# Performance work log

Measured on AMD Instinct MI355X. Metric: run time of the kernel, lower is better.

The kernel has to match this reference:

```python
import jax, jax.numpy as jnp
import numpy as np

B, N, D, D_A, S, D_K = 512, 8192, 1024, 512, 8, 64

def setup_inputs() -> dict:
    key = jax.random.key(0)
    k1, k2, k3, k4 = jax.random.split(key, 4)
    lecun_q = 1.0 / np.sqrt(D_A)
    lecun_k = 1.0 / np.sqrt(D)
    return {
        "z": jax.random.normal(k1, (B, D_A), dtype=jnp.float32),
        "pool_vectors": jax.random.normal(k2, (N, D), dtype=jnp.float32),
        "W_Q": jax.random.normal(k3, (S, D_A, D_K), dtype=jnp.float32) * lecun_q,
        "W_K": jax.random.normal(k4, (S, D, D_K), dtype=jnp.float32) * lecun_k,
        "aspect_logits": jnp.zeros((S,), dtype=jnp.float32),
        "tau": jnp.asarray(0.5, dtype=jnp.float32),
        "lambda_sharp": jnp.asarray(10.0, dtype=jnp.float32),
        "temperature": jnp.asarray(0.1, dtype=jnp.float32),
    }

def reference(z, pool_vectors, W_Q, W_K, aspect_logits, tau, lambda_sharp, temperature):
    # Per-aspect projections
    queries = jnp.einsum('bd,adq->baq', z, W_Q)              # [B, S, d_k]
    keys = jnp.einsum('np,apq->naq', pool_vectors, W_K)       # [N, S, d_k]
    # L2 normalize along d_k
    q_norm = queries / (jnp.linalg.norm(queries, axis=-1, keepdims=True) + 1e-08)
    k_norm = keys / (jnp.linalg.norm(keys, axis=-1, keepdims=True) + 1e-08)
    # Multi-aspect cosine similarity
    sims = jnp.einsum('baq,naq->bna', q_norm, k_norm)          # [B, N, S]
    # Learned aspect weighting
    w = jax.nn.softmax(aspect_logits)                          # [S]
    scores = jnp.einsum('bna,a->bn', sims, w)                  # [B, N]
    # Sigmoid gate against threshold, temperature-scaled normalize
    g = jax.nn.sigmoid(lambda_sharp * (scores - tau))
    alpha_raw = g * jnp.exp(scores / temperature)
    alpha = alpha_raw / (jnp.sum(alpha_raw, axis=-1, keepdims=True) + 1e-08)
    return (alpha, scores, keys)
```

## Files before the change

### kernel.cpp

```cpp
#include <hip/hip_runtime.h>
#include <stdint.h>

#define B_DIM 512
#define N_DIM 8192
#define D_DIM 1024
#define DA_DIM 512
#define S_DIM 8
#define DK_DIM 64
#define C_DIM 512

typedef short v8s __attribute__((ext_vector_type(8)));
typedef float v4f __attribute__((ext_vector_type(4)));

__device__ __forceinline__ unsigned int f2bf(float x) {
    union { float f; unsigned int u; } v; v.f = x;
    unsigned int u = v.u;
    return (u + 0x7fffu + ((u >> 16) & 1u)) >> 16;
}

__device__ __forceinline__ void gld16(const unsigned short* g, unsigned short* l) {
    __builtin_amdgcn_global_load_lds(
        (const __attribute__((address_space(1))) unsigned int*)g,
        (__attribute__((address_space(3))) unsigned int*)l,
        16, 0, 0);
}

__device__ __forceinline__ void cvt8(const float* __restrict__ src,
                                     unsigned short* __restrict__ dst, int t) {
    const float4* s4 = (const float4*)src;
    float4 a = s4[2 * t], b = s4[2 * t + 1];
    uint4 o;
    o.x = f2bf(a.x) | (f2bf(a.y) << 16);
    o.y = f2bf(a.z) | (f2bf(a.w) << 16);
    o.z = f2bf(b.x) | (f2bf(b.y) << 16);
    o.w = f2bf(b.z) | (f2bf(b.w) << 16);
    ((uint4*)dst)[t] = o;
}

__device__ __forceinline__ void w_transpose_tile(const float* __restrict__ w,
                                                 unsigned short* __restrict__ wt,
                                                 int a, int dt, int ddim,
                                                 unsigned short* T ) {
    int t = threadIdx.x;
    int d0 = dt * 64;
    int kc4 = (t & 15) * 4;
    const float4* src = (const float4*)(w + ((size_t)a * ddim + d0) * DK_DIM);
    #pragma unroll
    for (int p = 0; p < 4; p++) {
        int dr = p * 16 + (t >> 4);
        float4 v = src[dr * 16 + (t & 15)];
        uint2 pk;
        pk.x = f2bf(v.x) | (f2bf(v.y) << 16);
        pk.y = f2bf(v.z) | (f2bf(v.w) << 16);
        *(uint2*)&T[dr * 68 + kc4] = pk;
    }
    __syncthreads();
    int c0 = a * 64;
    #pragma unroll
    for (int q = 0; q < 2; q++) {
        int k = q * 32 + (t >> 3);
        int ch = t & 7;
        unsigned short s[8];
        #pragma unroll
        for (int i = 0; i < 8; i++) s[i] = T[(ch * 8 + i) * 68 + k];
        uint4 o;
        o.x = (unsigned)s[0] | ((unsigned)s[1] << 16);
        o.y = (unsigned)s[2] | ((unsigned)s[3] << 16);
        o.z = (unsigned)s[4] | ((unsigned)s[5] << 16);
        o.w = (unsigned)s[6] | ((unsigned)s[7] << 16);
        *(uint4*)&wt[(size_t)(c0 + k) * ddim + d0 + ch * 8] = o;
    }
}

__global__ __launch_bounds__(256) void prep(const float* __restrict__ pool,
                                            const float* __restrict__ z,
                                            const float* __restrict__ W_Q,
                                            const float* __restrict__ W_K,
                                            unsigned short* __restrict__ poolb,
                                            unsigned short* __restrict__ zb,
                                            unsigned short* __restrict__ wqt,
                                            unsigned short* __restrict__ wtb) {
    __shared__ unsigned short T[64 * 68];
    int blk = blockIdx.x;
    if (blk < 4096) {
        cvt8(pool, poolb, blk * 256 + threadIdx.x);
    } else if (blk < 4224) {
        cvt8(z, zb, (blk - 4096) * 256 + threadIdx.x);
    } else if (blk < 4352) {
        int idx = blk - 4224;
        w_transpose_tile(W_K, wtb, idx >> 4, idx & 15, D_DIM, T);
    } else {
        int idx = blk - 4352;
        w_transpose_tile(W_Q, wqt, idx >> 3, idx & 7, DA_DIM, T);
    }
}

__device__ __forceinline__ void gemm_mainloop(const unsigned short* __restrict__ A, int lda,
                                              const unsigned short* __restrict__ Bm, int ldb,
                                              int mbase, int nbase, int kiters64,
                                              unsigned short (*As)[2][4096],
                                              unsigned short (*Bs)[2][2048],
                                              v4f acc[2][4]) {
    int tid = threadIdx.x;
    int wid = tid >> 6, lane = tid & 63;
    int quad = lane >> 4, l16 = lane & 15;
    int srow = lane >> 2;
    int scol = (lane & 3) * 8;

    auto stage = [&](int kk, int p) {
        int k0 = kk * 64;
        #pragma unroll
        for (int j = 0; j < 6; j++) {
            int i = wid * 6 + j;
            if (i < 16) {
                int c = i >> 3, g = i & 7;
                int row = g * 16 + srow;
                gld16(&A[(size_t)(mbase + row) * lda + k0 + c * 32 + scol],
                      &As[p][c][g * 512]);
            } else {
                int i2 = i - 16;
                int c = i2 >> 2, g = i2 & 3;
                int row = g * 16 + srow;
                gld16(&Bm[(size_t)(nbase + row) * ldb + k0 + c * 32 + scol],
                      &Bs[p][c][g * 512]);
            }
        }
    };

    stage(0, 0);
    for (int kk = 0; kk < kiters64; kk++) {
        __syncthreads();
        if (kk + 1 < kiters64) stage(kk + 1, (kk + 1) & 1);
        int p = kk & 1;
        #pragma unroll
        for (int c = 0; c < 2; c++) {
            v8s af[2], bf[4];
            #pragma unroll
            for (int mt = 0; mt < 2; mt++)
                af[mt] = *(const v8s*)&As[p][c][(wid * 32 + mt * 16 + l16) * 32 + quad * 8];
            #pragma unroll
            for (int nt = 0; nt < 4; nt++)
                bf[nt] = *(const v8s*)&Bs[p][c][(nt * 16 + l16) * 32 + quad * 8];
            #pragma unroll
            for (int mt = 0; mt < 2; mt++)
                #pragma unroll
                for (int nt = 0; nt < 4; nt++)
                    acc[mt][nt] = __builtin_amdgcn_mfma_f32_16x16x32_bf16(
                        af[mt], bf[nt], acc[mt][nt], 0, 0, 0);
        }
    }
}

__global__ __launch_bounds__(256, 3) void fused_gemms(const unsigned short* __restrict__ poolb,
                                                      const unsigned short* __restrict__ wtb,
                                                      const unsigned short* __restrict__ zb,
                                                      const unsigned short* __restrict__ wqt,
                                                      const float* __restrict__ logits,
                                                      float* __restrict__ keys_out,
                                                      unsigned short* __restrict__ kb,
                                                      unsigned short* __restrict__ qwb) {
    __shared__ unsigned short As[2][2][4096];
    __shared__ unsigned short Bs[2][2][2048];
    v4f acc[2][4];
    #pragma unroll
    for (int mt = 0; mt < 2; mt++)
        #pragma unroll
        for (int nt = 0; nt < 4; nt++) acc[mt][nt] = (v4f)(0.f);

    int blk = blockIdx.x;
    bool is_q = blk >= 512;
    int mbase, nbase;
    if (is_q) {
        int q = blk - 512;
        mbase = (q & 3) * 128; nbase = (q >> 2) * 64;
        gemm_mainloop(zb, DA_DIM, wqt, DA_DIM, mbase, nbase, DA_DIM / 64, As, Bs, acc);
    } else {
        mbase = (blk & 63) * 128; nbase = (blk >> 6) * 64;
        gemm_mainloop(poolb, D_DIM, wtb, D_DIM, mbase, nbase, D_DIM / 64, As, Bs, acc);
    }

    int tid = threadIdx.x, wid = tid >> 6, lane = tid & 63;
    int quad = lane >> 4, l16 = lane & 15;

    if (is_q) {
        float l[8]; float mx = -1e30f;
        #pragma unroll
        for (int i = 0; i < 8; i++) { l[i] = logits[i]; mx = fmaxf(mx, l[i]); }
        float se = 0.f;
        #pragma unroll
        for (int i = 0; i < 8; i++) { l[i] = __expf(l[i] - mx); se += l[i]; }
        float wa = l[nbase >> 6] / se;

        #pragma unroll
        for (int mt = 0; mt < 2; mt++)
            #pragma unroll
            for (int r = 0; r < 4; r++) {
                float ss = 0.f;
                #pragma unroll
                for (int nt = 0; nt < 4; nt++) ss += acc[mt][nt][r] * acc[mt][nt][r];
                ss += __shfl_xor(ss, 1, 64);
                ss += __shfl_xor(ss, 2, 64);
                ss += __shfl_xor(ss, 4, 64);
                ss += __shfl_xor(ss, 8, 64);
                float sc = wa / (sqrtf(ss) + 1e-8f);
                int row = mbase + wid * 32 + mt * 16 + quad * 4 + r;
                #pragma unroll
                for (int nt = 0; nt < 4; nt++) {
                    int col = nbase + nt * 16 + l16;
                    qwb[(size_t)row * C_DIM + col] =
                        (unsigned short)f2bf(acc[mt][nt][r] * sc);
                }
            }
    } else {
        #pragma unroll
        for (int mt = 0; mt < 2; mt++)
            #pragma unroll
            for (int r = 0; r < 4; r++) {
                float ss = 0.f;
                #pragma unroll
                for (int nt = 0; nt < 4; nt++) ss += acc[mt][nt][r] * acc[mt][nt][r];
                ss += __shfl_xor(ss, 1, 64);
                ss += __shfl_xor(ss, 2, 64);
                ss += __shfl_xor(ss, 4, 64);
                ss += __shfl_xor(ss, 8, 64);
                float sc = 1.0f / (sqrtf(ss) + 1e-8f);
                int row = mbase + wid * 32 + mt * 16 + quad * 4 + r;
                #pragma unroll
                for (int nt = 0; nt < 4; nt++) {
                    int col = nbase + nt * 16 + l16;
                    float s = acc[mt][nt][r];
                    keys_out[(size_t)row * C_DIM + col] = s;
                    kb[(size_t)row * C_DIM + col] = (unsigned short)f2bf(s * sc);
                }
            }
    }
}

__global__ __launch_bounds__(256, 3) void scores_gemm(const unsigned short* __restrict__ qwb,
                                                      const unsigned short* __restrict__ kb,
                                                      float* __restrict__ scores_out,
                                                      float* __restrict__ partials,
                                                      const float* __restrict__ lam_p,
                                                      const float* __restrict__ tau_p,
                                                      const float* __restrict__ temp_p) {
    __shared__ unsigned short As[2][2][4096];
    __shared__ unsigned short Bs[2][2][2048];
    __shared__ float rowpart[128];
    v4f acc[2][4];
    #pragma unroll
    for (int mt = 0; mt < 2; mt++)
        #pragma unroll
        for (int nt = 0; nt < 4; nt++) acc[mt][nt] = (v4f)(0.f);

    int mbase = blockIdx.y * 128, nbase = blockIdx.x * 64;
    gemm_mainloop(qwb, C_DIM, kb, C_DIM, mbase, nbase, C_DIM / 64, As, Bs, acc);

    int tid = threadIdx.x, wid = tid >> 6, lane = tid & 63;
    int quad = lane >> 4, l16 = lane & 15;

    float lam = lam_p[0], tau = tau_p[0], invT = 1.0f / temp_p[0];

    #pragma unroll
    for (int mt = 0; mt < 2; mt++)
        #pragma unroll
        for (int r = 0; r < 4; r++) {
            float rs = 0.f;
            int row = mbase + wid * 32 + mt * 16 + quad * 4 + r;
            #pragma unroll
            for (int nt = 0; nt < 4; nt++) {
                float s = acc[mt][nt][r];
                int col = nbase + nt * 16 + l16;
                scores_out[(size_t)row * N_DIM + col] = s;
                float g = 1.0f / (1.0f + __expf(-lam * (s - tau)));
                rs += g * __expf(s * invT);
            }
            rs += __shfl_xor(rs, 1, 64);
            rs += __shfl_xor(rs, 2, 64);
            rs += __shfl_xor(rs, 4, 64);
            rs += __shfl_xor(rs, 8, 64);
            if (l16 == 0)
                rowpart[wid * 32 + mt * 16 + quad * 4 + r] = rs;
        }
    __syncthreads();
    if (tid < 128)
        partials[(size_t)blockIdx.x * B_DIM + mbase + tid] = rowpart[tid];
}

__global__ __launch_bounds__(256) void alpha_kernel(const float* __restrict__ scores,
                                                    const float* __restrict__ partials,
                                                    float* __restrict__ alpha,
                                                    const float* __restrict__ lam_p,
                                                    const float* __restrict__ tau_p,
                                                    const float* __restrict__ temp_p) {
    __shared__ float red[128];
    __shared__ float s_inv;
    int b = blockIdx.x >> 1;
    int half = blockIdx.x & 1;
    int tid = threadIdx.x;
    if (tid < 128) red[tid] = partials[(size_t)tid * B_DIM + b];
    __syncthreads();
    if (tid < 64) {
        float v = red[tid] + red[tid + 64];
        v += __shfl_xor(v, 1, 64);
        v += __shfl_xor(v, 2, 64);
        v += __shfl_xor(v, 4, 64);
        v += __shfl_xor(v, 8, 64);
        v += __shfl_xor(v, 16, 64);
        v += __shfl_xor(v, 32, 64);
        if (tid == 0) s_inv = 1.0f / (v + 1e-8f);
    }
    __syncthreads();
    float inv = s_inv;
    float lam = lam_p[0], tau = tau_p[0], invT = 1.0f / temp_p[0];
    const float4* srow = (const float4*)(scores + (size_t)b * N_DIM) + half * 1024;
    float4* arow = (float4*)(alpha + (size_t)b * N_DIM) + half * 1024;
    #pragma unroll
    for (int i = 0; i < 4; i++) {
        int idx = tid + i * 256;
        float4 s4 = srow[idx];
        float4 o;
        o.x = (1.0f / (1.0f + __expf(-lam * (s4.x - tau)))) * __expf(s4.x * invT) * inv;
        o.y = (1.0f / (1.0f + __expf(-lam * (s4.y - tau)))) * __expf(s4.y * invT) * inv;
        o.z = (1.0f / (1.0f + __expf(-lam * (s4.z - tau)))) * __expf(s4.z * invT) * inv;
        o.w = (1.0f / (1.0f + __expf(-lam * (s4.w - tau)))) * __expf(s4.w * invT) * inv;
        arow[idx] = o;
    }
}

extern "C" void kernel_launch(void* const* d_in, const int* in_sizes, int n_in,
                              void* d_out, int out_size, void* d_ws, size_t ws_size,
                              hipStream_t stream) {
    const float* z      = (const float*)d_in[0];
    const float* pool   = (const float*)d_in[1];
    const float* W_Q    = (const float*)d_in[2];
    const float* W_K    = (const float*)d_in[3];
    const float* logits = (const float*)d_in[4];
    const float* tau    = (const float*)d_in[5];
    const float* lam    = (const float*)d_in[6];
    const float* temp   = (const float*)d_in[7];

    float* alpha  = (float*)d_out;
    float* scores = alpha + (size_t)B_DIM * N_DIM;
    float* keys   = scores + (size_t)B_DIM * N_DIM;

    char* ws = (char*)d_ws;
    unsigned short* poolb = (unsigned short*)(ws);
    unsigned short* kb    = (unsigned short*)(ws + 16777216);
    unsigned short* wtb   = (unsigned short*)(ws + 25165824);
    unsigned short* wqt   = (unsigned short*)(ws + 26214400);
    unsigned short* zb    = (unsigned short*)(ws + 26738688);
    unsigned short* qwb   = (unsigned short*)(ws + 27262976);
    float* partials       = (float*)(ws + 27787264);

    prep<<<dim3(4416), dim3(256), 0, stream>>>(pool, z, W_Q, W_K,
                                               poolb, zb, wqt, wtb);
    fused_gemms<<<dim3(544), dim3(256), 0, stream>>>(poolb, wtb, zb, wqt, logits,
                                                     keys, kb, qwb);
    scores_gemm<<<dim3(128, 4), dim3(256), 0, stream>>>(qwb, kb, scores, partials,
                                                        lam, tau, temp);
    alpha_kernel<<<dim3(1024), dim3(256), 0, stream>>>(scores, partials, alpha,
                                                       lam, tau, temp);
}
```

Baseline: 138.5 us.

## Fuse pool fp32-to-bf16 conversion into key GEMM A-tile loading

The separate prep pass that converted the 32MB fp32 pool into a bf16 workspace copy is removed. The key-projection GEMM now loads fp32 pool tiles into registers, converts them to bf16, and writes them to LDS, prefetching the next tile during the MFMA loop. This drops a full write and re-read of the bf16 pool. In exchange the GEMM reads twice as many bytes per A tile, uses more registers, and does conversion ALU work inside the main loop, while the pool is re-read by each of the 8 N-column blocks.

Result: slower. 158.1 us (+14.1%).

```diff
diff --git a/kernel.cpp b/kernel.cpp
--- a/kernel.cpp
+++ b/kernel.cpp
@@ -72,25 +72,21 @@
     }
 }
 
-__global__ __launch_bounds__(256) void prep(const float* __restrict__ pool,
-                                            const float* __restrict__ z,
+__global__ __launch_bounds__(256) void prep(const float* __restrict__ z,
                                             const float* __restrict__ W_Q,
                                             const float* __restrict__ W_K,
-                                            unsigned short* __restrict__ poolb,
                                             unsigned short* __restrict__ zb,
                                             unsigned short* __restrict__ wqt,
                                             unsigned short* __restrict__ wtb) {
     __shared__ unsigned short T[64 * 68];
     int blk = blockIdx.x;
-    if (blk < 4096) {
-        cvt8(pool, poolb, blk * 256 + threadIdx.x);
-    } else if (blk < 4224) {
-        cvt8(z, zb, (blk - 4096) * 256 + threadIdx.x);
-    } else if (blk < 4352) {
-        int idx = blk - 4224;
+    if (blk < 128) {
+        cvt8(z, zb, blk * 256 + threadIdx.x);
+    } else if (blk < 256) {
+        int idx = blk - 128;
         w_transpose_tile(W_K, wtb, idx >> 4, idx & 15, D_DIM, T);
     } else {
-        int idx = blk - 4352;
+        int idx = blk - 256;
         w_transpose_tile(W_Q, wqt, idx >> 3, idx & 7, DA_DIM, T);
     }
 }
@@ -151,7 +147,82 @@
     }
 }
 
-__global__ __launch_bounds__(256, 3) void fused_gemms(const unsigned short* __restrict__ poolb,
+__device__ __forceinline__ void gemm_mainloop_cvtA(const float* __restrict__ Af,
+                                                   const unsigned short* __restrict__ Bm,
+                                                   int mbase, int nbase, int kiters64,
+                                                   unsigned short (*As)[2][4096],
+                                                   unsigned short (*Bs)[2][2048],
+                                                   v4f acc[2][4]) {
+    int tid = threadIdx.x;
+    int wid = tid >> 6, lane = tid & 63;
+    int quad = lane >> 4, l16 = lane & 15;
+    int srow = lane >> 2;
+    int scol = (lane & 3) * 8;
+
+    float4 fa[4][2];
+
+    auto issueA = [&](int kk) {
+        #pragma unroll
+        for (int j = 0; j < 4; j++) {
+            int u = wid * 4 + j;
+            int c = u >> 3, g = u & 7;
+            int row = g * 16 + srow;
+            const float* p = Af + (size_t)(mbase + row) * D_DIM + kk * 64 + c * 32 + scol;
+            fa[j][0] = *(const float4*)p;
+            fa[j][1] = *(const float4*)(p + 4);
+        }
+    };
+    auto commitA = [&](int pb) {
+        #pragma unroll
+        for (int j = 0; j < 4; j++) {
+            int u = wid * 4 + j;
+            int c = u >> 3, g = u & 7;
+            uint4 o;
+            o.x = f2bf(fa[j][0].x) | (f2bf(fa[j][0].y) << 16);
+            o.y = f2bf(fa[j][0].z) | (f2bf(fa[j][0].w) << 16);
+            o.z = f2bf(fa[j][1].x) | (f2bf(fa[j][1].y) << 16);
+            o.w = f2bf(fa[j][1].z) | (f2bf(fa[j][1].w) << 16);
+            *(uint4*)&As[pb][c][g * 512 + lane * 8] = o;
+        }
+    };
+    auto gldB = [&](int kk, int pb) {
+        #pragma unroll
+        for (int j = 0; j < 2; j++) {
+            int u = wid * 2 + j;
+            int c = u >> 2, g = u & 3;
+            int row = g * 16 + srow;
+            gld16(&Bm[(size_t)(nbase + row) * D_DIM + kk * 64 + c * 32 + scol],
+                  &Bs[pb][c][g * 512]);
+        }
+    };
+
+    issueA(0); gldB(0, 0); commitA(0);
+    for (int kk = 0; kk < kiters64; kk++) {
+        __syncthreads();
+        int pn = (kk + 1) & 1;
+        if (kk + 1 < kiters64) { issueA(kk + 1); gldB(kk + 1, pn); }
+        int p = kk & 1;
+        #pragma unroll
+        for (int c = 0; c < 2; c++) {
+            v8s af[2], bf[4];
+            #pragma unroll
+            for (int mt = 0; mt < 2; mt++)
+                af[mt] = *(const v8s*)&As[p][c][(wid * 32 + mt * 16 + l16) * 32 + quad * 8];
+            #pragma unroll
+            for (int nt = 0; nt < 4; nt++)
+                bf[nt] = *(const v8s*)&Bs[p][c][(nt * 16 + l16) * 32 + quad * 8];
+            #pragma unroll
+            for (int mt = 0; mt < 2; mt++)
+                #pragma unroll
+                for (int nt = 0; nt < 4; nt++)
+                    acc[mt][nt] = __builtin_amdgcn_mfma_f32_16x16x32_bf16(
+                        af[mt], bf[nt], acc[mt][nt], 0, 0, 0);
+        }
+        if (kk + 1 < kiters64) commitA(pn);
+    }
+}
+
+__global__ __launch_bounds__(256, 3) void fused_gemms(const float* __restrict__ pool,
                                                       const unsigned short* __restrict__ wtb,
                                                       const unsigned short* __restrict__ zb,
                                                       const unsigned short* __restrict__ wqt,
@@ -176,7 +247,7 @@
         gemm_mainloop(zb, DA_DIM, wqt, DA_DIM, mbase, nbase, DA_DIM / 64, As, Bs, acc);
     } else {
         mbase = (blk & 63) * 128; nbase = (blk >> 6) * 64;
-        gemm_mainloop(poolb, D_DIM, wtb, D_DIM, mbase, nbase, D_DIM / 64, As, Bs, acc);
+        gemm_mainloop_cvtA(pool, wtb, mbase, nbase, D_DIM / 64, As, Bs, acc);
     }
 
     int tid = threadIdx.x, wid = tid >> 6, lane = tid & 63;
@@ -344,17 +415,15 @@
     float* keys   = scores + (size_t)B_DIM * N_DIM;
 
     char* ws = (char*)d_ws;
-    unsigned short* poolb = (unsigned short*)(ws);
-    unsigned short* kb    = (unsigned short*)(ws + 16777216);
-    unsigned short* wtb   = (unsigned short*)(ws + 25165824);
-    unsigned short* wqt   = (unsigned short*)(ws + 26214400);
-    unsigned short* zb    = (unsigned short*)(ws + 26738688);
-    unsigned short* qwb   = (unsigned short*)(ws + 27262976);
-    float* partials       = (float*)(ws + 27787264);
-
-    prep<<<dim3(4416), dim3(256), 0, stream>>>(pool, z, W_Q, W_K,
-                                               poolb, zb, wqt, wtb);
-    fused_gemms<<<dim3(544), dim3(256), 0, stream>>>(poolb, wtb, zb, wqt, logits,
+    unsigned short* kb  = (unsigned short*)(ws);
+    unsigned short* wtb = (unsigned short*)(ws + 8388608);
+    unsigned short* wqt = (unsigned short*)(ws + 9437184);
+    unsigned short* zb  = (unsigned short*)(ws + 9961472);
+    unsigned short* qwb = (unsigned short*)(ws + 10485760);
+    float* partials     = (float*)(ws + 11010048);
+
+    prep<<<dim3(320), dim3(256), 0, stream>>>(z, W_Q, W_K, zb, wqt, wtb);
+    fused_gemms<<<dim3(544), dim3(256), 0, stream>>>(pool, wtb, zb, wqt, logits,
                                                      keys, kb, qwb);
     scores_gemm<<<dim3(128, 4), dim3(256), 0, stream>>>(qwb, kb, scores, partials,
                                                         lam, tau, temp);
```

## Enlarge GEMM block tiles to 128x128 with a 2x2 warp layout

Applied to the files above, without the earlier changes.

Both GEMM kernels now use 128x128 output tiles split across four waves in a 2x2 grid, each wave holding a 64x64 accumulator (4x4 MFMA tiles). The grids are halved, occupancy is lowered to 2 blocks per CU, and the scores kernel merges the two column-halves of each row sum with shared-memory atomics. The alpha kernel now reads 64 partials per row instead of 128. The aim is more MFMA work per LDS fragment load and fewer global loads per FLOP. The cost is higher register pressure, fewer blocks (272 and 256) to fill the CUs, and less latency hiding.

After: 140.4 us. About the same (+1.4%).

```diff
diff --git a/kernel.cpp b/kernel.cpp
--- a/kernel.cpp
+++ b/kernel.cpp
@@ -99,10 +99,11 @@
                                               const unsigned short* __restrict__ Bm, int ldb,
                                               int mbase, int nbase, int kiters64,
                                               unsigned short (*As)[2][4096],
-                                              unsigned short (*Bs)[2][2048],
-                                              v4f acc[2][4]) {
+                                              unsigned short (*Bs)[2][4096],
+                                              v4f acc[4][4]) {
     int tid = threadIdx.x;
     int wid = tid >> 6, lane = tid & 63;
+    int wm = wid >> 1, wn = wid & 1;
     int quad = lane >> 4, l16 = lane & 15;
     int srow = lane >> 2;
     int scol = (lane & 3) * 8;
@@ -110,20 +111,16 @@
     auto stage = [&](int kk, int p) {
         int k0 = kk * 64;
         #pragma unroll
-        for (int j = 0; j < 6; j++) {
-            int i = wid * 6 + j;
-            if (i < 16) {
-                int c = i >> 3, g = i & 7;
-                int row = g * 16 + srow;
+        for (int j = 0; j < 8; j++) {
+            int i = wid * 8 + j;
+            int c = (i >> 3) & 1, g = i & 7;
+            int row = g * 16 + srow;
+            if (i < 16)
                 gld16(&A[(size_t)(mbase + row) * lda + k0 + c * 32 + scol],
                       &As[p][c][g * 512]);
-            } else {
-                int i2 = i - 16;
-                int c = i2 >> 2, g = i2 & 3;
-                int row = g * 16 + srow;
+            else
                 gld16(&Bm[(size_t)(nbase + row) * ldb + k0 + c * 32 + scol],
                       &Bs[p][c][g * 512]);
-            }
         }
     };
 
@@ -134,15 +131,15 @@
         int p = kk & 1;
         #pragma unroll
         for (int c = 0; c < 2; c++) {
-            v8s af[2], bf[4];
-            #pragma unroll
-            for (int mt = 0; mt < 2; mt++)
-                af[mt] = *(const v8s*)&As[p][c][(wid * 32 + mt * 16 + l16) * 32 + quad * 8];
+            v8s af[4], bf[4];
+            #pragma unroll
+            for (int mt = 0; mt < 4; mt++)
+                af[mt] = *(const v8s*)&As[p][c][(wm * 64 + mt * 16 + l16) * 32 + quad * 8];
             #pragma unroll
             for (int nt = 0; nt < 4; nt++)
-                bf[nt] = *(const v8s*)&Bs[p][c][(nt * 16 + l16) * 32 + quad * 8];
-            #pragma unroll
-            for (int mt = 0; mt < 2; mt++)
+                bf[nt] = *(const v8s*)&Bs[p][c][(wn * 64 + nt * 16 + l16) * 32 + quad * 8];
+            #pragma unroll
+            for (int mt = 0; mt < 4; mt++)
                 #pragma unroll
                 for (int nt = 0; nt < 4; nt++)
                     acc[mt][nt] = __builtin_amdgcn_mfma_f32_16x16x32_bf16(
@@ -151,7 +148,7 @@
     }
 }
 
-__global__ __launch_bounds__(256, 3) void fused_gemms(const unsigned short* __restrict__ poolb,
+__global__ __launch_bounds__(256, 2) void fused_gemms(const unsigned short* __restrict__ poolb,
                                                       const unsigned short* __restrict__ wtb,
                                                       const unsigned short* __restrict__ zb,
                                                       const unsigned short* __restrict__ wqt,
@@ -160,27 +157,27 @@
                                                       unsigned short* __restrict__ kb,
                                                       unsigned short* __restrict__ qwb) {
     __shared__ unsigned short As[2][2][4096];
-    __shared__ unsigned short Bs[2][2][2048];
-    v4f acc[2][4];
-    #pragma unroll
-    for (int mt = 0; mt < 2; mt++)
+    __shared__ unsigned short Bs[2][2][4096];
+    v4f acc[4][4];
+    #pragma unroll
+    for (int mt = 0; mt < 4; mt++)
         #pragma unroll
         for (int nt = 0; nt < 4; nt++) acc[mt][nt] = (v4f)(0.f);
 
     int blk = blockIdx.x;
-    bool is_q = blk >= 512;
+    bool is_q = blk >= 256;
     int mbase, nbase;
     if (is_q) {
-        int q = blk - 512;
-        mbase = (q & 3) * 128; nbase = (q >> 2) * 64;
+        int q = blk - 256;
+        mbase = (q & 3) * 128; nbase = (q >> 2) * 128;
         gemm_mainloop(zb, DA_DIM, wqt, DA_DIM, mbase, nbase, DA_DIM / 64, As, Bs, acc);
     } else {
-        mbase = (blk & 63) * 128; nbase = (blk >> 6) * 64;
+        mbase = (blk & 63) * 128; nbase = (blk >> 6) * 128;
         gemm_mainloop(poolb, D_DIM, wtb, D_DIM, mbase, nbase, D_DIM / 64, As, Bs, acc);
     }
 
     int tid = threadIdx.x, wid = tid >> 6, lane = tid & 63;
-    int quad = lane >> 4, l16 = lane & 15;
+    int wm = wid >> 1, wn = wid & 1, quad = lane >> 4, l16 = lane & 15;
 
     if (is_q) {
         float l[8]; float mx = -1e30f;
@@ -189,10 +186,10 @@
         float se = 0.f;
         #pragma unroll
         for (int i = 0; i < 8; i++) { l[i] = __expf(l[i] - mx); se += l[i]; }
-        float wa = l[nbase >> 6] / se;
-
-        #pragma unroll
-        for (int mt = 0; mt < 2; mt++)
+        float wa = l[(nbase >> 6) + wn] / se;
+
+        #pragma unroll
+        for (int mt = 0; mt < 4; mt++)
             #pragma unroll
             for (int r = 0; r < 4; r++) {
                 float ss = 0.f;
@@ -203,17 +200,17 @@
                 ss += __shfl_xor(ss, 4, 64);
                 ss += __shfl_xor(ss, 8, 64);
                 float sc = wa / (sqrtf(ss) + 1e-8f);
-                int row = mbase + wid * 32 + mt * 16 + quad * 4 + r;
+                int row = mbase + wm * 64 + mt * 16 + quad * 4 + r;
                 #pragma unroll
                 for (int nt = 0; nt < 4; nt++) {
-                    int col = nbase + nt * 16 + l16;
+                    int col = nbase + wn * 64 + nt * 16 + l16;
                     qwb[(size_t)row * C_DIM + col] =
                         (unsigned short)f2bf(acc[mt][nt][r] * sc);
                 }
             }
     } else {
         #pragma unroll
-        for (int mt = 0; mt < 2; mt++)
+        for (int mt = 0; mt < 4; mt++)
             #pragma unroll
             for (int r = 0; r < 4; r++) {
                 float ss = 0.f;
@@ -224,10 +221,10 @@
                 ss += __shfl_xor(ss, 4, 64);
                 ss += __shfl_xor(ss, 8, 64);
                 float sc = 1.0f / (sqrtf(ss) + 1e-8f);
-                int row = mbase + wid * 32 + mt * 16 + quad * 4 + r;
+                int row = mbase + wm * 64 + mt * 16 + quad * 4 + r;
                 #pragma unroll
                 for (int nt = 0; nt < 4; nt++) {
-                    int col = nbase + nt * 16 + l16;
+                    int col = nbase + wn * 64 + nt * 16 + l16;
                     float s = acc[mt][nt][r];
                     keys_out[(size_t)row * C_DIM + col] = s;
                     kb[(size_t)row * C_DIM + col] = (unsigned short)f2bf(s * sc);
@@ -236,7 +233,7 @@
     }
 }
 
-__global__ __launch_bounds__(256, 3) void scores_gemm(const unsigned short* __restrict__ qwb,
+__global__ __launch_bounds__(256, 2) void scores_gemm(const unsigned short* __restrict__ qwb,
                                                       const unsigned short* __restrict__ kb,
                                                       float* __restrict__ scores_out,
                                                       float* __restrict__ partials,
@@ -244,32 +241,35 @@
                                                       const float* __restrict__ tau_p,
                                                       const float* __restrict__ temp_p) {
     __shared__ unsigned short As[2][2][4096];
-    __shared__ unsigned short Bs[2][2][2048];
+    __shared__ unsigned short Bs[2][2][4096];
     __shared__ float rowpart[128];
-    v4f acc[2][4];
-    #pragma unroll
-    for (int mt = 0; mt < 2; mt++)
+    v4f acc[4][4];
+    #pragma unroll
+    for (int mt = 0; mt < 4; mt++)
         #pragma unroll
         for (int nt = 0; nt < 4; nt++) acc[mt][nt] = (v4f)(0.f);
 
-    int mbase = blockIdx.y * 128, nbase = blockIdx.x * 64;
+    int mbase = blockIdx.y * 128, nbase = blockIdx.x * 128;
     gemm_mainloop(qwb, C_DIM, kb, C_DIM, mbase, nbase, C_DIM / 64, As, Bs, acc);
 
     int tid = threadIdx.x, wid = tid >> 6, lane = tid & 63;
-    int quad = lane >> 4, l16 = lane & 15;
+    int wm = wid >> 1, wn = wid & 1, quad = lane >> 4, l16 = lane & 15;
+
+    if (tid < 128) rowpart[tid] = 0.f;
+    __syncthreads();
 
     float lam = lam_p[0], tau = tau_p[0], invT = 1.0f / temp_p[0];
 
     #pragma unroll
-    for (int mt = 0; mt < 2; mt++)
+    for (int mt = 0; mt < 4; mt++)
         #pragma unroll
         for (int r = 0; r < 4; r++) {
             float rs = 0.f;
-            int row = mbase + wid * 32 + mt * 16 + quad * 4 + r;
+            int row = mbase + wm * 64 + mt * 16 + quad * 4 + r;
             #pragma unroll
             for (int nt = 0; nt < 4; nt++) {
                 float s = acc[mt][nt][r];
-                int col = nbase + nt * 16 + l16;
+                int col = nbase + wn * 64 + nt * 16 + l16;
                 scores_out[(size_t)row * N_DIM + col] = s;
                 float g = 1.0f / (1.0f + __expf(-lam * (s - tau)));
                 rs += g * __expf(s * invT);
@@ -279,7 +279,7 @@
             rs += __shfl_xor(rs, 4, 64);
             rs += __shfl_xor(rs, 8, 64);
             if (l16 == 0)
-                rowpart[wid * 32 + mt * 16 + quad * 4 + r] = rs;
+                atomicAdd(&rowpart[wm * 64 + mt * 16 + quad * 4 + r], rs);
         }
     __syncthreads();
     if (tid < 128)
@@ -292,15 +292,12 @@
                                                     const float* __restrict__ lam_p,
                                                     const float* __restrict__ tau_p,
                                                     const float* __restrict__ temp_p) {
-    __shared__ float red[128];
     __shared__ float s_inv;
     int b = blockIdx.x >> 1;
     int half = blockIdx.x & 1;
     int tid = threadIdx.x;
-    if (tid < 128) red[tid] = partials[(size_t)tid * B_DIM + b];
-    __syncthreads();
     if (tid < 64) {
-        float v = red[tid] + red[tid + 64];
+        float v = partials[(size_t)tid * B_DIM + b];
         v += __shfl_xor(v, 1, 64);
         v += __shfl_xor(v, 2, 64);
         v += __shfl_xor(v, 4, 64);
@@ -354,10 +351,10 @@
 
     prep<<<dim3(4416), dim3(256), 0, stream>>>(pool, z, W_Q, W_K,
                                                poolb, zb, wqt, wtb);
-    fused_gemms<<<dim3(544), dim3(256), 0, stream>>>(poolb, wtb, zb, wqt, logits,
+    fused_gemms<<<dim3(272), dim3(256), 0, stream>>>(poolb, wtb, zb, wqt, logits,
                                                      keys, kb, qwb);
-    scores_gemm<<<dim3(128, 4), dim3(256), 0, stream>>>(qwb, kb, scores, partials,
-                                                        lam, tau, temp);
+    scores_gemm<<<dim3(64, 4), dim3(256), 0, stream>>>(qwb, kb, scores, partials,
+                                                       lam, tau, temp);
     alpha_kernel<<<dim3(1024), dim3(256), 0, stream>>>(scores, partials, alpha,
                                                        lam, tau, temp);
 }
```
